# Kernel tuning notes

Measured on AMD Instinct MI355X. Metric: run time of the kernel, lower is better.

## Reference

```python
import jax, jax.numpy as jnp
import numpy as np

N_USERS = 50000
N_ITEMS = 50000
E = 400000
S = 128   # in_feats_s (memory / GRU hidden)
T = 64    # in_feats_t (time encoding dim)
ED = 64   # edge feature dim
M = 2 * S + T + ED  # in_feats_m = 384

_BASIS_FREQ = jnp.asarray(1.0 / 10 ** np.linspace(0, 9, T), dtype=jnp.float32)


def time_encode(ts):
    # cos(ts * freq + phase), phase == 0
    return jnp.cos(ts[:, None] * _BASIS_FREQ[None, :])


def mean_message(src_mem, dst_mem, ts, e, src, dst, n_dst):
    # mail per edge: [E, 2S + T + ED]
    mail = jnp.concatenate(
        [src_mem[src], dst_mem[dst], time_encode(ts), e], axis=1)
    s = jax.ops.segment_sum(mail, dst, num_segments=n_dst)
    cnt = jax.ops.segment_sum(jnp.ones_like(ts), dst, num_segments=n_dst)
    return s / jnp.maximum(cnt, 1.0)[:, None]


def gru_step(x, h, w_ih, w_hh, b_ih, b_hh):
    # single-step PyTorch GRU; gate order r, z, n
    gi = x @ w_ih.T + b_ih
    gh = h @ w_hh.T + b_hh
    ir, iz, i_n = jnp.split(gi, 3, axis=1)
    hr, hz, h_n = jnp.split(gh, 3, axis=1)
    r = jax.nn.sigmoid(ir + hr)
    z = jax.nn.sigmoid(iz + hz)
    n = jnp.tanh(i_n + r * h_n)
    return (1.0 - z) * n + z * h


def setup_inputs() -> dict:
    key = jax.random.key(0)
    ks = jax.random.split(key, 16)
    sc = 1.0 / np.sqrt(S)
    return {
        "si":   jax.random.normal(ks[0], (N_USERS, S), jnp.float32),
        "sj":   jax.random.normal(ks[1], (N_ITEMS, S), jnp.float32),
        "si_r": jax.random.normal(ks[2], (N_ITEMS, S), jnp.float32),
        "sj_r": jax.random.normal(ks[3], (N_USERS, S), jnp.float32),
        "t":    jax.random.uniform(ks[4], (E,), jnp.float32),
        "t_r":  jax.random.uniform(ks[5], (E,), jnp.float32),
        "e":    jax.random.normal(ks[6], (E, ED), jnp.float32),
        "e_r":  jax.random.normal(ks[7], (E, ED), jnp.float32),
        "w_ih": jax.random.normal(ks[8], (3 * S, M), jnp.float32) * sc,
        "w_hh": jax.random.normal(ks[9], (3 * S, S), jnp.float32) * sc,
        "b_ih": jax.random.normal(ks[10], (3 * S,), jnp.float32) * sc,
        "b_hh": jax.random.normal(ks[11], (3 * S,), jnp.float32) * sc,
        "src_g":  jax.random.randint(ks[12], (E,), 0, N_USERS, jnp.int32),
        "dst_g":  jax.random.randint(ks[13], (E,), 0, N_ITEMS, jnp.int32),
        "src_gr": jax.random.randint(ks[14], (E,), 0, N_ITEMS, jnp.int32),
        "dst_gr": jax.random.randint(ks[15], (E,), 0, N_USERS, jnp.int32),
    }


def reference(si, sj, si_r, sj_r, t, t_r, e, e_r,
              w_ih, w_hh, b_ih, b_hh,
              src_g, dst_g, src_gr, dst_gr):
    # g: user -> item; g_r: item -> user
    mj = mean_message(si, sj, t, e, src_g, dst_g, N_ITEMS)       # messages to items
    mi = mean_message(si_r, sj_r, t_r, e_r, src_gr, dst_gr, N_USERS)  # messages to users
    si_out = gru_step(mi, sj_r, w_ih, w_hh, b_ih, b_hh)  # user memory update
    sj_out = gru_step(mj, sj, w_ih, w_hh, b_ih, b_hh)    # item memory update
    return (si_out, sj_out)
```

## Files before the change

kernel.cpp:

```cpp
#include <hip/hip_runtime.h>
#include <math.h>

#define NUSERS 50000
#define NITEMS 50000
#define NTOT   100000
#define NNODE  50000
#define NCHUNK 196
#define MTILES 6250
#define KDIM   512

typedef __attribute__((ext_vector_type(4))) float f32x4;
typedef __attribute__((ext_vector_type(8))) short short8;
typedef unsigned int u32;

#define AS1 __attribute__((address_space(1)))
#define AS3 __attribute__((address_space(3)))

static __device__ __forceinline__ unsigned short f2bf(float f) {
  unsigned int u = __float_as_uint(f);
  u += 0x7fffu + ((u >> 16) & 1u);
  return (unsigned short)(u >> 16);
}

static __device__ __forceinline__ u32 pack2(float x, float y) {
  return (u32)f2bf(x) | ((u32)f2bf(y) << 16);
}

static __device__ __forceinline__ void gload_lds16(const void* g, void* l) {
  __builtin_amdgcn_global_load_lds((const AS1 u32*)g, (AS3 u32*)l, 16, 0, 0);
}

__global__ void pack_w_kernel(const float* __restrict__ w_ih,
                              const float* __restrict__ w_hh,
                              const float* __restrict__ b_ih,
                              const float* __restrict__ b_hh,
                              unsigned short* __restrict__ Wb,
                              float* __restrict__ bb) {
  int idx = blockIdx.x * 256 + threadIdx.x;
  int j = idx & 7, l = (idx >> 3) & 63, ktt = idx >> 9;
  int kt = ktt & 15, tt = ktt >> 4;
  int g = tt * 16 + (l & 15);
  int k = kt * 32 + (l >> 4) * 8 + j;
  float v;
  if (g < 256)      v = (k < 384) ? w_ih[g * 384 + k] : w_hh[g * 128 + (k - 384)];
  else if (g < 384) v = (k < 384) ? w_ih[g * 384 + k] : 0.0f;
  else              v = (k < 384) ? 0.0f : w_hh[(g - 128) * 128 + (k - 384)];
  Wb[idx] = f2bf(v);
  if (idx < 512) {
    float b = (idx < 256) ? (b_ih[idx] + b_hh[idx])
            : (idx < 384) ? b_ih[idx]
                          : b_hh[idx - 128];
    bb[idx] = b;
  }
}

__global__ void cast_mem_kernel(const float* __restrict__ si,
                                const float* __restrict__ si_r,
                                unsigned short* __restrict__ si_b,
                                unsigned short* __restrict__ sir_b) {
  int i = blockIdx.x * 256 + threadIdx.x;
  const float* src; unsigned short* dst; int off;
  if (i < 800000) { src = si;   dst = si_b;  off = i; }
  else            { src = si_r; dst = sir_b; off = i - 800000; }
  const f32x4* p = (const f32x4*)(src + (size_t)off * 8);
  f32x4 a = p[0], b = p[1];
  short8 o;
  o[0] = f2bf(a[0]); o[1] = f2bf(a[1]); o[2] = f2bf(a[2]); o[3] = f2bf(a[3]);
  o[4] = f2bf(b[0]); o[5] = f2bf(b[1]); o[6] = f2bf(b[2]); o[7] = f2bf(b[3]);
  *(short8*)(dst + (size_t)off * 8) = o;
}

__global__ void hist_kernel(const int* __restrict__ dst_g,
                            const int* __restrict__ dst_gr,
                            int* __restrict__ deg_j, int* __restrict__ deg_i, int E) {
  int i = blockIdx.x * 256 + threadIdx.x;
  if (i < E) atomicAdd(&deg_j[dst_g[i]], 1);
  else if (i < 2 * E) atomicAdd(&deg_i[dst_gr[i - E]], 1);
}

__global__ void chunksum_kernel(const int* __restrict__ deg_j,
                                const int* __restrict__ deg_i,
                                int* __restrict__ csum) {
  int c = blockIdx.x;
  const int* deg = (c < NCHUNK) ? deg_j : deg_i;
  int cc = (c < NCHUNK) ? c : c - NCHUNK;
  int t = threadIdx.x;
  int idx = cc * 256 + t;
  int v = (idx < NNODE) ? deg[idx] : 0;
  for (int off = 32; off; off >>= 1) v += __shfl_down(v, off, 64);
  __shared__ int wsum[4];
  if ((t & 63) == 0) wsum[t >> 6] = v;
  __syncthreads();
  if (t == 0) csum[c] = wsum[0] + wsum[1] + wsum[2] + wsum[3];
}

__global__ void chunkscan_kernel(const int* __restrict__ csum, int* __restrict__ coff) {
  int d = blockIdx.x;
  const int* cs = csum + d * NCHUNK;
  int* co = coff + d * NCHUNK;
  int t = threadIdx.x, lane = t & 63, w = t >> 6;
  int v = (t < NCHUNK) ? cs[t] : 0;
  int x = v;
  for (int off = 1; off < 64; off <<= 1) {
    int y = __shfl_up(x, off, 64);
    if (lane >= off) x += y;
  }
  __shared__ int wt[4];
  if (lane == 63) wt[w] = x;
  __syncthreads();
  int add = 0;
  for (int k = 0; k < 4; ++k) if (k < w) add += wt[k];
  if (t < NCHUNK) co[t] = add + x - v;
}

__global__ void localscan_kernel(const int* __restrict__ deg_j,
                                 const int* __restrict__ deg_i,
                                 const int* __restrict__ coff,
                                 int* __restrict__ rs_j, int* __restrict__ cur_j,
                                 int* __restrict__ rs_i, int* __restrict__ cur_i) {
  int c = blockIdx.x;
  bool dj = c < NCHUNK;
  const int* deg = dj ? deg_j : deg_i;
  int cc = dj ? c : c - NCHUNK;
  int* rs = dj ? rs_j : rs_i;
  int* cur = dj ? cur_j : cur_i;
  int base = coff[c];
  int t = threadIdx.x, lane = t & 63, w = t >> 6;
  int idx = cc * 256 + t;
  int v = (idx < NNODE) ? deg[idx] : 0;
  int x = v;
  for (int off = 1; off < 64; off <<= 1) {
    int y = __shfl_up(x, off, 64);
    if (lane >= off) x += y;
  }
  __shared__ int wt[4];
  if (lane == 63) wt[w] = x;
  __syncthreads();
  int add = 0;
  for (int k = 0; k < 4; ++k) if (k < w) add += wt[k];
  int ex = base + add + x - v;
  if (idx < NNODE) { rs[idx] = ex; cur[idx] = ex; }
}

__global__ void fill_kernel(const int* __restrict__ src_g, const int* __restrict__ dst_g,
                            const float* __restrict__ t,
                            const int* __restrict__ src_gr, const int* __restrict__ dst_gr,
                            const float* __restrict__ t_r,
                            int* __restrict__ cur_j, int* __restrict__ cur_i,
                            int4* __restrict__ recP_j, int4* __restrict__ recP_i,
                            int E) {
  int i = blockIdx.x * 256 + threadIdx.x;
  if (i < E) {
    int pos = atomicAdd(&cur_j[dst_g[i]], 1);
    recP_j[pos] = make_int4(src_g[i], i, __float_as_int(t[i]), 0);
  } else if (i < 2 * E) {
    int k = i - E;
    int pos = atomicAdd(&cur_i[dst_gr[k]], 1);
    recP_i[pos] = make_int4(src_gr[k], k, __float_as_int(t_r[k]), 0);
  }
}

__global__ __launch_bounds__(256) void gather_kernel(
    const unsigned short* __restrict__ si_b, const unsigned short* __restrict__ sir_b,
    const float* __restrict__ sj, const float* __restrict__ sj_r,
    const float* __restrict__ e, const float* __restrict__ e_r,
    const int* __restrict__ rs_j, const int* __restrict__ rs_i,
    const int* __restrict__ deg_j, const int* __restrict__ deg_i,
    const int4* __restrict__ recP_j, const int4* __restrict__ recP_i,
    unsigned short* __restrict__ Xb) {
  __shared__ __align__(16) unsigned short rowbuf[4][512];
  int wid = threadIdx.x >> 6, lane = threadIdx.x & 63;
  int node = blockIdx.x * 4 + wid;
  bool user = node < NUSERS;
  int idx = user ? node : node - NUSERS;
  const unsigned short* smem = user ? sir_b : si_b;
  const float* h    = user ? sj_r : sj;
  const float* ef   = user ? e_r : e;
  int start = __builtin_amdgcn_readfirstlane((user ? rs_i : rs_j)[idx]);
  int deg   = __builtin_amdgcn_readfirstlane((user ? deg_i : deg_j)[idx]);
  const int4* rec = user ? recP_i : recP_j;

  float freq = __expf((float)lane * -0.3289407276f);
  float2 hvf = *(const float2*)(h + (size_t)idx * 128 + 2 * lane);

  float asx = 0.f, asy = 0.f;
  float at  = 0.f;
  float ae  = 0.f;

  for (int base = 0; base < deg; base += 64) {
    int nn = deg - base; if (nn > 64) nn = 64;
    int cl = (lane < nn) ? base + lane : base + nn - 1;
    int4 r = rec[start + cl];
    for (int j0 = 0; j0 < nn; j0 += 8) {
      int j1 = (j0 + 1 < nn) ? j0 + 1 : nn - 1;
      int j2 = (j0 + 2 < nn) ? j0 + 2 : nn - 1;
      int j3 = (j0 + 3 < nn) ? j0 + 3 : nn - 1;
      int j4 = (j0 + 4 < nn) ? j0 + 4 : nn - 1;
      int j5 = (j0 + 5 < nn) ? j0 + 5 : nn - 1;
      int j6 = (j0 + 6 < nn) ? j0 + 6 : nn - 1;
      int j7 = (j0 + 7 < nn) ? j0 + 7 : nn - 1;
      float w1 = (j0 + 1 < nn) ? 1.0f : 0.0f;
      float w2 = (j0 + 2 < nn) ? 1.0f : 0.0f;
      float w3 = (j0 + 3 < nn) ? 1.0f : 0.0f;
      float w4 = (j0 + 4 < nn) ? 1.0f : 0.0f;
      float w5 = (j0 + 5 < nn) ? 1.0f : 0.0f;
      float w6 = (j0 + 6 < nn) ? 1.0f : 0.0f;
      float w7 = (j0 + 7 < nn) ? 1.0f : 0.0f;

      int s0 = __builtin_amdgcn_readlane(r.x, j0), e0 = __builtin_amdgcn_readlane(r.y, j0);
      int s1 = __builtin_amdgcn_readlane(r.x, j1), e1 = __builtin_amdgcn_readlane(r.y, j1);
      int s2 = __builtin_amdgcn_readlane(r.x, j2), e2 = __builtin_amdgcn_readlane(r.y, j2);
      int s3 = __builtin_amdgcn_readlane(r.x, j3), e3 = __builtin_amdgcn_readlane(r.y, j3);
      int s4 = __builtin_amdgcn_readlane(r.x, j4), e4 = __builtin_amdgcn_readlane(r.y, j4);
      int s5 = __builtin_amdgcn_readlane(r.x, j5), e5 = __builtin_amdgcn_readlane(r.y, j5);
      int s6 = __builtin_amdgcn_readlane(r.x, j6), e6 = __builtin_amdgcn_readlane(r.y, j6);
      int s7 = __builtin_amdgcn_readlane(r.x, j7), e7 = __builtin_amdgcn_readlane(r.y, j7);

      u32 v0 = *(const u32*)(smem + ((size_t)s0 << 7) + 2 * lane);
      u32 v1 = *(const u32*)(smem + ((size_t)s1 << 7) + 2 * lane);
      u32 v2 = *(const u32*)(smem + ((size_t)s2 << 7) + 2 * lane);
      u32 v3 = *(const u32*)(smem + ((size_t)s3 << 7) + 2 * lane);
      u32 v4 = *(const u32*)(smem + ((size_t)s4 << 7) + 2 * lane);
      u32 v5 = *(const u32*)(smem + ((size_t)s5 << 7) + 2 * lane);
      u32 v6 = *(const u32*)(smem + ((size_t)s6 << 7) + 2 * lane);
      u32 v7 = *(const u32*)(smem + ((size_t)s7 << 7) + 2 * lane);
      float f0 = ef[((size_t)e0 << 6) + lane];
      float f1 = ef[((size_t)e1 << 6) + lane];
      float f2 = ef[((size_t)e2 << 6) + lane];
      float f3 = ef[((size_t)e3 << 6) + lane];
      float f4 = ef[((size_t)e4 << 6) + lane];
      float f5 = ef[((size_t)e5 << 6) + lane];
      float f6 = ef[((size_t)e6 << 6) + lane];
      float f7 = ef[((size_t)e7 << 6) + lane];

      float c0 = __cosf(__int_as_float(__builtin_amdgcn_readlane(r.z, j0)) * freq);
      float c1 = __cosf(__int_as_float(__builtin_amdgcn_readlane(r.z, j1)) * freq);
      float c2 = __cosf(__int_as_float(__builtin_amdgcn_readlane(r.z, j2)) * freq);
      float c3 = __cosf(__int_as_float(__builtin_amdgcn_readlane(r.z, j3)) * freq);
      float c4 = __cosf(__int_as_float(__builtin_amdgcn_readlane(r.z, j4)) * freq);
      float c5 = __cosf(__int_as_float(__builtin_amdgcn_readlane(r.z, j5)) * freq);
      float c6 = __cosf(__int_as_float(__builtin_amdgcn_readlane(r.z, j6)) * freq);
      float c7 = __cosf(__int_as_float(__builtin_amdgcn_readlane(r.z, j7)) * freq);

      float l0 = __uint_as_float(v0 << 16), g0 = __uint_as_float(v0 & 0xffff0000u);
      float l1 = __uint_as_float(v1 << 16), g1 = __uint_as_float(v1 & 0xffff0000u);
      float l2 = __uint_as_float(v2 << 16), g2 = __uint_as_float(v2 & 0xffff0000u);
      float l3 = __uint_as_float(v3 << 16), g3 = __uint_as_float(v3 & 0xffff0000u);
      float l4 = __uint_as_float(v4 << 16), g4 = __uint_as_float(v4 & 0xffff0000u);
      float l5 = __uint_as_float(v5 << 16), g5 = __uint_as_float(v5 & 0xffff0000u);
      float l6 = __uint_as_float(v6 << 16), g6 = __uint_as_float(v6 & 0xffff0000u);
      float l7 = __uint_as_float(v7 << 16), g7 = __uint_as_float(v7 & 0xffff0000u);

      asx += l0 + w1 * l1 + w2 * l2 + w3 * l3 + w4 * l4 + w5 * l5 + w6 * l6 + w7 * l7;
      asy += g0 + w1 * g1 + w2 * g2 + w3 * g3 + w4 * g4 + w5 * g5 + w6 * g6 + w7 * g7;
      at  += c0 + w1 * c1 + w2 * c2 + w3 * c3 + w4 * c4 + w5 * c5 + w6 * c6 + w7 * c7;
      ae  += f0 + w1 * f1 + w2 * f2 + w3 * f3 + w4 * f4 + w5 * f5 + w6 * f6 + w7 * f7;
    }
  }

  float invc = (deg > 0) ? 1.0f / (float)deg : 0.0f;
  float hz   = (deg > 0) ? 1.0f : 0.0f;

  unsigned short* rb = rowbuf[wid];
  u32* rb32 = (u32*)rb;
  rb32[lane]       = pack2(asx * invc, asy * invc);
  rb32[64 + lane]  = pack2(hvf.x * hz, hvf.y * hz);
  rb[256 + lane]   = f2bf(at * invc);
  rb[320 + lane]   = f2bf(ae * invc);
  rb32[192 + lane] = pack2(hvf.x, hvf.y);

  int rt = node >> 4, m = node & 15;
  int kt2 = lane >> 2, q2 = lane & 3;
  short8 vv = *(const short8*)(rb + lane * 8);
  *(short8*)(Xb + (((size_t)rt * 16 + kt2) * 64 + q2 * 16 + m) * 8) = vv;
}

__global__ __launch_bounds__(512, 2) void gemm_gru_kernel(
    const unsigned short* __restrict__ Xb,
    const unsigned short* __restrict__ Wb,
    const float* __restrict__ bb,
    const float* __restrict__ sj_r,
    const float* __restrict__ sj,
    float* __restrict__ out) {
  __shared__ __align__(16) unsigned short sB[32768];
  int wid = threadIdx.x >> 6, lane = threadIdx.x & 63;
  int mtile = blockIdx.x * 8 + wid;
  bool valid = mtile < MTILES;
  int col16 = lane & 15, quad = lane >> 4;

  f32x4 acc[32];
#pragma unroll
  for (int t = 0; t < 32; ++t) acc[t] = (f32x4)0.0f;

  const unsigned short* Abase = Xb + (size_t)(valid ? mtile : 0) * 8192;

  for (int s = 0; s < 8; ++s) {
#pragma unroll
    for (int i = 0; i < 8; ++i) {
      int c = wid * 8 + i;
      int tt = c >> 1, kt = s * 2 + (c & 1);
      const unsigned short* g = Wb + ((size_t)(tt * 16 + kt) * 64 + lane) * 8;
      gload_lds16(g, sB + c * 512);
    }
    __syncthreads();
    if (valid) {
      short8 a0 = *(const short8*)(Abase + (size_t)(s * 2) * 512 + lane * 8);
      short8 a1 = *(const short8*)(Abase + (size_t)(s * 2 + 1) * 512 + lane * 8);
#pragma unroll
      for (int t = 0; t < 32; ++t) {
        short8 b0 = *(const short8*)(sB + (t * 2) * 512 + lane * 8);
        short8 b1 = *(const short8*)(sB + (t * 2 + 1) * 512 + lane * 8);
        acc[t] = __builtin_amdgcn_mfma_f32_16x16x32_bf16(a0, b0, acc[t], 0, 0, 0);
        acc[t] = __builtin_amdgcn_mfma_f32_16x16x32_bf16(a1, b1, acc[t], 0, 0, 0);
      }
    }
    __syncthreads();
  }

  if (!valid) return;
  int m0 = mtile * 16;
#pragma unroll
  for (int t = 0; t < 8; ++t) {
    int c = t * 16 + col16;
    float bbr = bb[c], bbz = bb[128 + c], bbn = bb[256 + c], bbh = bb[384 + c];
#pragma unroll
    for (int r = 0; r < 4; ++r) {
      int row = m0 + quad * 4 + r;
      float rp  = acc[t][r]      + bbr;
      float zp  = acc[t + 8][r]  + bbz;
      float inp = acc[t + 16][r] + bbn;
      float hnp = acc[t + 24][r] + bbh;
      float rg = 1.0f / (1.0f + __expf(-rp));
      float zg = 1.0f / (1.0f + __expf(-zp));
      float ng = tanhf(inp + rg * hnp);
      float hv = (row < NUSERS) ? sj_r[(size_t)row * 128 + c]
                                : sj[(size_t)(row - NUSERS) * 128 + c];
      out[(size_t)row * 128 + c] = (1.0f - zg) * ng + zg * hv;
    }
  }
}

extern "C" void kernel_launch(void* const* d_in, const int* in_sizes, int n_in,
                              void* d_out, int out_size, void* d_ws, size_t ws_size,
                              hipStream_t stream) {
  const float* si   = (const float*)d_in[0];
  const float* sj   = (const float*)d_in[1];
  const float* si_r = (const float*)d_in[2];
  const float* sj_r = (const float*)d_in[3];
  const float* t    = (const float*)d_in[4];
  const float* t_r  = (const float*)d_in[5];
  const float* e    = (const float*)d_in[6];
  const float* e_r  = (const float*)d_in[7];
  const float* w_ih = (const float*)d_in[8];
  const float* w_hh = (const float*)d_in[9];
  const float* b_ih = (const float*)d_in[10];
  const float* b_hh = (const float*)d_in[11];
  const int* src_g  = (const int*)d_in[12];
  const int* dst_g  = (const int*)d_in[13];
  const int* src_gr = (const int*)d_in[14];
  const int* dst_gr = (const int*)d_in[15];
  int E = in_sizes[4];

  unsigned short* Xb = (unsigned short*)d_ws;
  unsigned short* Wb = Xb + (size_t)MTILES * 8192;
  float* bb   = (float*)(Wb + 262144);
  int* deg_j  = (int*)(bb + 512);
  int* deg_i  = deg_j + NNODE;
  int* rs_j   = deg_i + NNODE;
  int* rs_i   = rs_j + NNODE;
  int* cur_j  = rs_i + NNODE;
  int* cur_i  = cur_j + NNODE;
  int* csum   = cur_i + NNODE;
  int* coff   = csum + 2 * NCHUNK;
  int4* recP_j = (int4*)(coff + 2 * NCHUNK);
  int4* recP_i = recP_j + E;
  unsigned short* si_b  = (unsigned short*)(recP_i + E);
  unsigned short* sir_b = si_b + 6400000;

  hipMemsetAsync(deg_j, 0, 2 * NNODE * sizeof(int), stream);

  pack_w_kernel<<<(512 * 512) / 256, 256, 0, stream>>>(w_ih, w_hh, b_ih, b_hh, Wb, bb);
  cast_mem_kernel<<<6250, 256, 0, stream>>>(si, si_r, si_b, sir_b);

  int blks2E = (2 * E + 255) / 256;
  hist_kernel<<<blks2E, 256, 0, stream>>>(dst_g, dst_gr, deg_j, deg_i, E);
  chunksum_kernel<<<2 * NCHUNK, 256, 0, stream>>>(deg_j, deg_i, csum);
  chunkscan_kernel<<<2, 256, 0, stream>>>(csum, coff);
  localscan_kernel<<<2 * NCHUNK, 256, 0, stream>>>(deg_j, deg_i, coff, rs_j, cur_j, rs_i, cur_i);
  fill_kernel<<<blks2E, 256, 0, stream>>>(src_g, dst_g, t, src_gr, dst_gr, t_r,
                                          cur_j, cur_i, recP_j, recP_i, E);

  gather_kernel<<<NTOT / 4, 256, 0, stream>>>(si_b, sir_b, sj, sj_r, e, e_r,
                                              rs_j, rs_i, deg_j, deg_i,
                                              recP_j, recP_i, Xb);

  float* out = (float*)d_out;
  gemm_gru_kernel<<<(MTILES + 7) / 8, 512, 0, stream>>>(Xb, Wb, bb, sj_r, sj, out);
}
```

Before: 647.6 us.

## Split GEMM-GRU block by N columns and double-buffer weight tiles in LDS

Each block now covers 4 row tiles, and each wave owns a 16-column slice of all four gates instead of one row tile across all 512 columns. B fragments are held in registers and reused across the 4 M tiles, which cuts LDS reads per MFMA and the accumulator registers per wave (16 instead of 32 vectors). The weight staging is double-buffered so the next K slice loads while the current one is computed. The cost is twice the blocks, each restaging the full weight matrix, a doubled LDS footprint (128 KB) that likely limits occupancy, and A tiles now read redundantly by all 8 waves.

```diff
diff --git a/kernel.cpp b/kernel.cpp
--- a/kernel.cpp
+++ b/kernel.cpp
@@ -282,54 +282,71 @@
     const float* __restrict__ sj_r,
     const float* __restrict__ sj,
     float* __restrict__ out) {
-  __shared__ __align__(16) unsigned short sB[32768];
+  __shared__ __align__(16) unsigned short sB[2][32768];
   int wid = threadIdx.x >> 6, lane = threadIdx.x & 63;
-  int mtile = blockIdx.x * 8 + wid;
-  bool valid = mtile < MTILES;
+  int mbase = blockIdx.x * 4;
   int col16 = lane & 15, quad = lane >> 4;
 
-  f32x4 acc[32];
-#pragma unroll
-  for (int t = 0; t < 32; ++t) acc[t] = (f32x4)0.0f;
-
-  const unsigned short* Abase = Xb + (size_t)(valid ? mtile : 0) * 8192;
+  f32x4 acc[4][4];
+#pragma unroll
+  for (int mi = 0; mi < 4; ++mi)
+#pragma unroll
+    for (int g = 0; g < 4; ++g) acc[mi][g] = (f32x4)0.0f;
+
+#define STAGE(buf, s)                                                        \
+  {                                                                          \
+    _Pragma("unroll")                                                        \
+    for (int i = 0; i < 8; ++i) {                                            \
+      int c = wid * 8 + i;                                                   \
+      int tt = c >> 1, kt = (s) * 2 + (c & 1);                               \
+      const unsigned short* gp = Wb + ((size_t)(tt * 16 + kt) * 64 + lane) * 8; \
+      gload_lds16(gp, sB[buf] + c * 512);                                    \
+    }                                                                        \
+  }
+
+  STAGE(0, 0)
+  __syncthreads();
 
   for (int s = 0; s < 8; ++s) {
-#pragma unroll
-    for (int i = 0; i < 8; ++i) {
-      int c = wid * 8 + i;
-      int tt = c >> 1, kt = s * 2 + (c & 1);
-      const unsigned short* g = Wb + ((size_t)(tt * 16 + kt) * 64 + lane) * 8;
-      gload_lds16(g, sB + c * 512);
-    }
-    __syncthreads();
-    if (valid) {
-      short8 a0 = *(const short8*)(Abase + (size_t)(s * 2) * 512 + lane * 8);
-      short8 a1 = *(const short8*)(Abase + (size_t)(s * 2 + 1) * 512 + lane * 8);
-#pragma unroll
-      for (int t = 0; t < 32; ++t) {
-        short8 b0 = *(const short8*)(sB + (t * 2) * 512 + lane * 8);
-        short8 b1 = *(const short8*)(sB + (t * 2 + 1) * 512 + lane * 8);
-        acc[t] = __builtin_amdgcn_mfma_f32_16x16x32_bf16(a0, b0, acc[t], 0, 0, 0);
-        acc[t] = __builtin_amdgcn_mfma_f32_16x16x32_bf16(a1, b1, acc[t], 0, 0, 0);
+    int cur = s & 1;
+    if (s < 7) STAGE(cur ^ 1, s + 1)
+    short8 bfr[4][2];
+#pragma unroll
+    for (int g = 0; g < 4; ++g)
+#pragma unroll
+      for (int kp = 0; kp < 2; ++kp) {
+        int c = (g * 8 + wid) * 2 + kp;
+        bfr[g][kp] = *(const short8*)(sB[cur] + c * 512 + lane * 8);
+      }
+#pragma unroll
+    for (int mi = 0; mi < 4; ++mi) {
+      int mt = mbase + mi;
+      if (mt >= MTILES) mt = 0;
+      const unsigned short* Ab = Xb + (size_t)mt * 8192;
+      short8 a0 = *(const short8*)(Ab + (size_t)(s * 2) * 512 + lane * 8);
+      short8 a1 = *(const short8*)(Ab + (size_t)(s * 2 + 1) * 512 + lane * 8);
+#pragma unroll
+      for (int g = 0; g < 4; ++g) {
+        acc[mi][g] = __builtin_amdgcn_mfma_f32_16x16x32_bf16(a0, bfr[g][0], acc[mi][g], 0, 0, 0);
+        acc[mi][g] = __builtin_amdgcn_mfma_f32_16x16x32_bf16(a1, bfr[g][1], acc[mi][g], 0, 0, 0);
       }
     }
     __syncthreads();
   }
 
-  if (!valid) return;
-  int m0 = mtile * 16;
-#pragma unroll
-  for (int t = 0; t < 8; ++t) {
-    int c = t * 16 + col16;
-    float bbr = bb[c], bbz = bb[128 + c], bbn = bb[256 + c], bbh = bb[384 + c];
+  int c = wid * 16 + col16;
+  float bbr = bb[c], bbz = bb[128 + c], bbn = bb[256 + c], bbh = bb[384 + c];
+#pragma unroll
+  for (int mi = 0; mi < 4; ++mi) {
+    int mt = mbase + mi;
+    if (mt >= MTILES) continue;
 #pragma unroll
     for (int r = 0; r < 4; ++r) {
-      int row = m0 + quad * 4 + r;
-      float rp  = acc[t][r]      + bbr;
-      float zp  = acc[t + 8][r]  + bbz;
-      float inp = acc[t + 16][r] + bbn;
-      float hnp = acc[t + 24][r] + bbh;
+      int row = mt * 16 + quad * 4 + r;
+      float rp  = acc[mi][0][r] + bbr;
+      float zp  = acc[mi][1][r] + bbz;
+      float inp = acc[mi][2][r] + bbn;
+      float hnp = acc[mi][3][r] + bbh;
       float rg = 1.0f / (1.0f + __expf(-rp));
       float zg = 1.0f / (1.0f + __expf(-zp));
       float ng = tanhf(inp + rg * hnp);
@@ -395,5 +412,5 @@
                                               recP_j, recP_i, Xb);
 
   float* out = (float*)d_out;
-  gemm_gru_kernel<<<(MTILES + 7) / 8, 512, 0, stream>>>(Xb, Wb, bb, sj_r, sj, out);
-}
+  gemm_gru_kernel<<<(MTILES + 3) / 4, 512, 0, stream>>>(Xb, Wb, bb, sj_r, sj, out);
+}
```

Result: slower. 677.2 us (+4.6%).
